# Optimization experiments

Hardware: AMD Instinct MI355X
Metric: run time of the kernel (lower is better)

The kernel has to match this reference:

```python
import jax, jax.numpy as jnp
import numpy as np

B, T, C, H = 4, 2048, 1024, 16
HD = C // H


def setup_inputs() -> dict:
    key = jax.random.key(0)
    ks = jax.random.split(key, 9)
    s = 1.0 / np.sqrt(C)
    return {
        "x": jax.random.normal(ks[0], (B, T, C), dtype=jnp.float32),
        "Wk": jax.random.uniform(ks[1], (C, C), jnp.float32, -s, s),
        "bk": jax.random.uniform(ks[2], (C,), jnp.float32, -s, s),
        "Wq": jax.random.uniform(ks[3], (C, C), jnp.float32, -s, s),
        "bq": jax.random.uniform(ks[4], (C,), jnp.float32, -s, s),
        "Wv": jax.random.uniform(ks[5], (C, C), jnp.float32, -s, s),
        "bv": jax.random.uniform(ks[6], (C,), jnp.float32, -s, s),
        "Wp": jax.random.uniform(ks[7], (C, C), jnp.float32, -s, s),
        "bp": jax.random.uniform(ks[8], (C,), jnp.float32, -s, s),
        "padding_mask": jnp.ones((B, T), dtype=jnp.int32),
    }


def reference(x, Wk, bk, Wq, bq, Wv, bv, Wp, bp, padding_mask):
    # torch nn.Linear: y = x @ W.T + b  (W is [out, in])
    def split_heads(t):  # [B,T,C] -> [B,H,T,HD]
        return t.reshape(B, T, H, HD).transpose(0, 2, 1, 3)

    k = split_heads(x @ Wk.T + bk)
    q = split_heads(x @ Wq.T + bq)
    v = split_heads(x @ Wv.T + bv)

    scale = 1.0 / jnp.sqrt(jnp.float32(HD))
    att = jnp.einsum("bhqd,bhkd->bhqk", q, k) * scale  # [B,H,T,T]

    causal = jnp.tril(jnp.ones((T, T), dtype=bool))  # [T,T]
    pad = (padding_mask != 0)[:, None, None, :]       # [B,1,1,T]
    mask = causal[None, None, :, :] & pad
    att = jnp.where(mask, att, -jnp.inf)
    att = jax.nn.softmax(att, axis=-1)

    y = jnp.einsum("bhqk,bhkd->bhqd", att, v)  # [B,H,T,HD]
    y = y.transpose(0, 2, 1, 3).reshape(B, T, C)
    return y @ Wp.T + bp
```

## Files before the change

kernel.cpp:

```cpp
#include <hip/hip_runtime.h>
#include <hip/hip_bf16.h>
#include <math.h>
#include <stdint.h>

#define BB 4
#define TT 2048
#define CC 1024
#define HH 16
#define HD 64
#define MM (BB*TT)
#define NQT 16
#define SCQ 0.180336878f

using f32x4  = __attribute__((ext_vector_type(4))) float;
using bf16x4 = __attribute__((ext_vector_type(4))) __bf16;
using bf16x8 = __attribute__((ext_vector_type(8))) __bf16;

__device__ __forceinline__ float fast_exp2(float x) {
  return __builtin_amdgcn_exp2f(x);
}

__device__ __forceinline__ void gload_lds16(const void* g, void* l) {
  __builtin_amdgcn_global_load_lds(
      (__attribute__((address_space(1))) void*)(void*)(g),
      (__attribute__((address_space(3))) void*)(l), 16, 0, 0);
}

__global__ __launch_bounds__(256)
void cvt_f32_bf16(const float* __restrict__ s, __bf16* __restrict__ d, int n4) {
  int i = blockIdx.x * 256 + threadIdx.x;
  if (i >= n4) return;
  float4 v = ((const float4*)s)[i];
  bf16x4 o;
  o[0] = (__bf16)v.x; o[1] = (__bf16)v.y; o[2] = (__bf16)v.z; o[3] = (__bf16)v.w;
  *(bf16x4*)(d + (size_t)i * 4) = o;
}

__global__ __launch_bounds__(256)
void cvt_w4(const float* __restrict__ Wq, const float* __restrict__ Wk,
            const float* __restrict__ Wv, const float* __restrict__ Wp,
            __bf16* __restrict__ wqkv, __bf16* __restrict__ wpb) {
  int which = blockIdx.y;
  const float* s = which == 0 ? Wq : which == 1 ? Wk : which == 2 ? Wv : Wp;
  __bf16* d = which == 3 ? wpb : wqkv + (size_t)which * CC * CC;
  float sc = which == 0 ? SCQ : 1.f;
  int i = blockIdx.x * 256 + threadIdx.x;
  float4 v = ((const float4*)s)[i];
  bf16x4 o;
  o[0] = (__bf16)(v.x * sc); o[1] = (__bf16)(v.y * sc);
  o[2] = (__bf16)(v.z * sc); o[3] = (__bf16)(v.w * sc);
  *(bf16x4*)(d + (size_t)i * 4) = o;
}

#define WAITV6 asm volatile("s_waitcnt vmcnt(6)" ::: "memory")
#define WAITV0 asm volatile("s_waitcnt vmcnt(0)" ::: "memory")
#define WAITL0 asm volatile("s_waitcnt lgkmcnt(0)" ::: "memory")
#define BARR   __builtin_amdgcn_s_barrier()
#define SB0    __builtin_amdgcn_sched_barrier(0)
#define PRIO1  __builtin_amdgcn_s_setprio(1)
#define PRIO0  __builtin_amdgcn_s_setprio(0)

#define LDA_SET(buf, mq)                                                      \
  {                                                                           \
    const char* base_ = (const char*)&LA[buf][mq][0] + (wm * 64 + lq) * 128;  \
    _Pragma("unroll")                                                         \
    for (int m4 = 0; m4 < 4; ++m4)                                            \
      _Pragma("unroll")                                                       \
      for (int kk = 0; kk < 2; ++kk)                                          \
        a[m4 * 2 + kk] =                                                      \
            *(const bf16x8*)(base_ + m4 * 2048 + ((kk * 64 + g * 16) ^ swz)); \
  }

#define LDB_SET(buf, nq)                                                      \
  {                                                                           \
    const char* base_ = (const char*)&LB[buf][nq][0] + (wn * 32 + lq) * 128;  \
    _Pragma("unroll")                                                         \
    for (int n2 = 0; n2 < 2; ++n2)                                            \
      _Pragma("unroll")                                                       \
      for (int kk = 0; kk < 2; ++kk)                                          \
        b[nq][n2 * 2 + kk] =                                                  \
            *(const bf16x8*)(base_ + n2 * 2048 + ((kk * 64 + g * 16) ^ swz)); \
  }

#define STAGE_A(nbuf, h, tt)                                                  \
  {                                                                           \
    const char* s_ = Ag + ((size_t)((h)*128 + srow)) * 2048 + (tt)*128 + scol1; \
    gload_lds16(s_, (char*)&LA[nbuf][h][0] + so16);                           \
    gload_lds16(s_ + (size_t)64 * 2048, (char*)&LA[nbuf][h][0] + so16 + 8192);\
  }

#define STAGE_B(nbuf, h, tt)                                                  \
  {                                                                           \
    const char* s_ = Bg + ((size_t)((h)*128 + srow)) * 2048 + (tt)*128 + scol1; \
    gload_lds16(s_, (char*)&LB[nbuf][h][0] + so16);                           \
    gload_lds16(s_ + (size_t)64 * 2048, (char*)&LB[nbuf][h][0] + so16 + 8192);\
  }

#define MFMA_PH(mq, nq)                                                       \
  _Pragma("unroll")                                                           \
  for (int m4 = 0; m4 < 4; ++m4)                                              \
    _Pragma("unroll")                                                         \
    for (int n2 = 0; n2 < 2; ++n2)                                            \
      _Pragma("unroll")                                                       \
      for (int kk = 0; kk < 2; ++kk)                                          \
        acc[mq][m4][nq][n2] = __builtin_amdgcn_mfma_f32_16x16x32_bf16(        \
            a[m4 * 2 + kk], b[nq][n2 * 2 + kk], acc[mq][m4][nq][n2], 0, 0, 0);

__global__ __launch_bounds__(512, 2)
void gemm_qkv(const __bf16* __restrict__ A, const __bf16* __restrict__ Bm,
              const float* __restrict__ b0, const float* __restrict__ b1,
              const float* __restrict__ b2, __bf16* __restrict__ out,
              __bf16* __restrict__ vt) {
  __shared__ __bf16 LA[2][2][128 * 64];
  __shared__ __bf16 LB[2][2][128 * 64];
  const int tid = threadIdx.x, wid = tid >> 6, lane = tid & 63;
  const int g = lane >> 4, lq = lane & 15;
  const int wm = wid >> 2, wn = wid & 3;
  const int bm = blockIdx.x / 12, bn = blockIdx.x % 12;
  const int brow = bm << 8, bcol = bn << 8;
  const int swz = (lq & 7) << 4;

  const int srow = tid >> 3, so16 = tid * 16;
  const int scol1 = ((tid & 7) << 4) ^ ((srow & 7) << 4);
  const char* Ag = (const char*)A + (size_t)brow * 2048;
  const char* Bg = (const char*)Bm + (size_t)bcol * 2048;

  f32x4 acc[2][4][2][2] = {};
  bf16x8 a[8], b[2][4];

  STAGE_A(0, 0, 0); STAGE_B(0, 0, 0); STAGE_B(0, 1, 0); STAGE_A(0, 1, 0);
  STAGE_A(1, 0, 1); STAGE_B(1, 0, 1); STAGE_B(1, 1, 1);
  WAITV6; BARR;

#pragma unroll 1
  for (int t = 0; t < 8; ++t) {
    const bool s2 = (t < 7);
    const int k1 = 2 * t + 1, k2 = 2 * t + 2, k3 = 2 * t + 3;
    LDA_SET(0, 0); LDB_SET(0, 0);
    STAGE_A(1, 1, k1);
    BARR; WAITL0; SB0;
    PRIO1; MFMA_PH(0, 0); PRIO0; BARR;
    LDB_SET(0, 1);
    if (s2) STAGE_A(0, 0, k2);
    BARR; WAITL0; SB0;
    PRIO1; MFMA_PH(0, 1); PRIO0; BARR;
    LDA_SET(0, 1);
    if (s2) STAGE_B(0, 0, k2);
    BARR; WAITL0; SB0;
    PRIO1; MFMA_PH(1, 1); PRIO0; BARR;
    if (s2) { STAGE_B(0, 1, k2); WAITV6; } else { WAITV0; }
    BARR; SB0;
    PRIO1; MFMA_PH(1, 0); PRIO0; BARR;
    LDA_SET(1, 0); LDB_SET(1, 0);
    if (s2) STAGE_A(0, 1, k2);
    BARR; WAITL0; SB0;
    PRIO1; MFMA_PH(0, 0); PRIO0; BARR;
    LDB_SET(1, 1);
    if (s2) STAGE_A(1, 0, k3);
    BARR; WAITL0; SB0;
    PRIO1; MFMA_PH(0, 1); PRIO0; BARR;
    LDA_SET(1, 1);
    if (s2) STAGE_B(1, 0, k3);
    BARR; WAITL0; SB0;
    PRIO1; MFMA_PH(1, 1); PRIO0; BARR;
    if (s2) { STAGE_B(1, 1, k3); WAITV6; }
    BARR; SB0;
    PRIO1; MFMA_PH(1, 0); PRIO0; BARR;
  }

  const int proj = bn >> 2;
  if (proj < 2) {
    const float* bias = proj == 0 ? b0 : b1;
    const float bsc = proj == 0 ? SCQ : 1.f;
#pragma unroll
    for (int mq = 0; mq < 2; ++mq)
#pragma unroll
      for (int nq = 0; nq < 2; ++nq)
#pragma unroll
        for (int n2 = 0; n2 < 2; ++n2) {
          int col = bcol + nq * 128 + wn * 32 + n2 * 16 + lq;
          int cw = col & (CC - 1);
          float bb = bias[cw] * bsc;
          int h_ = cw >> 6, d_ = cw & (HD - 1);
#pragma unroll
          for (int m4 = 0; m4 < 4; ++m4) {
            int row0 = brow + mq * 128 + wm * 64 + m4 * 16 + g * 4;
#pragma unroll
            for (int i = 0; i < 4; ++i) {
              int row = row0 + i;
              int b_ = row >> 11, t_ = row & (TT - 1);
              out[((size_t)proj << 23) +
                  ((((size_t)b_ * HH + h_) * TT + t_) << 6) + d_] =
                  (__bf16)(acc[mq][m4][nq][n2][i] + bb);
            }
          }
        }
  } else {
    __bf16* lt = (__bf16*)&LA[0][0][0];
    const int cv0 = (bn & 3) << 8;
    const int b_ = brow >> 11, t0 = brow & (TT - 1);
    const int hbase = (bn & 3) << 2;
    const int rd_d = tid >> 3, rd_tb = (tid & 7) << 5;
#pragma unroll
    for (int cc = 0; cc < 4; ++cc) {
      if ((wn >> 1) == (cc & 1)) {
#pragma unroll
        for (int n2 = 0; n2 < 2; ++n2) {
          int c = ((wn & 1) << 5) + (n2 << 4) + lq;
          float bb = b2[cv0 + (cc << 6) + c];
#pragma unroll
          for (int mq = 0; mq < 2; ++mq)
#pragma unroll
            for (int m4 = 0; m4 < 4; ++m4) {
              int r = (mq << 7) + (wm << 6) + (m4 << 4) + (g << 2);
              bf16x4 pk;
#pragma unroll
              for (int i = 0; i < 4; ++i)
                pk[i] = (__bf16)(acc[mq][m4][cc >> 1][n2][i] + bb);
              *(bf16x4*)(lt + c * 264 + r) = pk;
            }
        }
      }
      __syncthreads();
      __bf16* dst = vt + (((size_t)((b_ * HH + hbase + cc) * HD + rd_d)) << 11)
                       + t0 + rd_tb;
      const __bf16* srcl = lt + rd_d * 264 + rd_tb;
#pragma unroll
      for (int j = 0; j < 4; ++j)
        *(bf16x8*)(dst + j * 8) = *(const bf16x8*)(srcl + j * 8);
      __syncthreads();
    }
  }
}

__global__ __launch_bounds__(256, 2)
void gemm_proj(const __bf16* __restrict__ A, const __bf16* __restrict__ Bm,
               const float* __restrict__ bias, float* __restrict__ out,
               int M, int N, int K) {
  __shared__ __bf16 As[128 * 32];
  __shared__ __bf16 Bs[128 * 32];
  const int tid = threadIdx.x;
  const int wid = tid >> 6, lane = tid & 63;
  const int g = lane >> 4, lq = lane & 15;
  const int nbn = N >> 7;
  const int brow = (blockIdx.x / nbn) << 7;
  const int bcol = (blockIdx.x % nbn) << 7;
  const int wr = (wid >> 1) << 6, wc = (wid & 1) << 6;

  f32x4 acc[4][4] = {};

  const int o0 = wid * 2048 + lane * 16;
  for (int kt = 0; kt < K; kt += 32) {
    __syncthreads();
#pragma unroll
    for (int j = 0; j < 2; ++j) {
      int o = o0 + j * 1024;
      int row = o >> 6, colb = o & 63;
      gload_lds16((const char*)A + ((size_t)(brow + row) * K + kt) * 2 + colb,
                  (char*)As + o);
      gload_lds16((const char*)Bm + ((size_t)(bcol + row) * K + kt) * 2 + colb,
                  (char*)Bs + o);
    }
    __syncthreads();
    bf16x8 av[4], bv[4];
#pragma unroll
    for (int m = 0; m < 4; ++m)
      av[m] = *(const bf16x8*)(As + (wr + m * 16 + lq) * 32 + g * 8);
#pragma unroll
    for (int n = 0; n < 4; ++n)
      bv[n] = *(const bf16x8*)(Bs + (wc + n * 16 + lq) * 32 + g * 8);
#pragma unroll
    for (int m = 0; m < 4; ++m)
#pragma unroll
      for (int n = 0; n < 4; ++n)
        acc[m][n] = __builtin_amdgcn_mfma_f32_16x16x32_bf16(av[m], bv[n], acc[m][n], 0, 0, 0);
  }

#pragma unroll
  for (int m = 0; m < 4; ++m) {
#pragma unroll
    for (int n = 0; n < 4; ++n) {
      int col = bcol + wc + n * 16 + lq;
      float bb = bias[col];
      int row0 = brow + wr + m * 16 + g * 4;
#pragma unroll
      for (int i = 0; i < 4; ++i)
        out[(size_t)(row0 + i) * N + col] = acc[m][n][i] + bb;
    }
  }
}

__global__ __launch_bounds__(512, 6)
void attn_fwd(const __bf16* __restrict__ Q, const __bf16* __restrict__ K,
              const __bf16* __restrict__ Vt, const int* __restrict__ pm,
              __bf16* __restrict__ Y) {
  __shared__ __bf16 Ks[2][64 * 64];
  __shared__ __bf16 Vs[2][64 * 64];
  __shared__ __bf16 Ps[8][16 * 72];
  const int tid = threadIdx.x, wid = tid >> 6, lane = tid & 63;
  const int g = lane >> 4, lq = lane & 15;
  const int bx = blockIdx.x;
  const int bh = bx & 63, jj = bx >> 6;
  const int qi = (jj & 1) ? ((jj - 1) >> 1) : (NQT - 1 - (jj >> 1));
  const int b_ = bh >> 4, h_ = bh & 15;
  const __bf16* Qb = Q + (size_t)bh * TT * HD;
  const __bf16* Kb = K + (size_t)bh * TT * HD;
  const __bf16* Vb = Vt + (size_t)bh * HD * TT;
  const int* pmb = pm + b_ * TT;

  const int so = tid * 16;
  const int srow = so >> 7, scol = (so & 127) ^ ((srow & 7) << 4);

  const int q0 = qi << 7;
  const int qw = q0 + wid * 16;
  const int ntiles = 2 * qi + 2;

  bf16x8 qf[2];
#pragma unroll
  for (int s = 0; s < 2; ++s)
    qf[s] = *(const bf16x8*)(Qb + (size_t)(qw + lq) * HD + s * 32 + g * 8);

  bf16x8 ones;
#pragma unroll
  for (int e = 0; e < 8; ++e) ones[e] = (__bf16)1.0f;

  f32x4 o[4] = {};
  f32x4 lacc = {0.f, 0.f, 0.f, 0.f};
  float mrow[4] = {-INFINITY, -INFINITY, -INFINITY, -INFINITY};

  gload_lds16((const char*)Kb + (size_t)srow * 128 + scol, (char*)&Ks[0][0] + so);
  gload_lds16((const char*)Vb + (size_t)srow * (TT * 2) + scol, (char*)&Vs[0][0] + so);
  __syncthreads();

  int cur = 0;
#pragma unroll 1
  for (int t = 0; t < ntiles; ++t) {
    const int kv0 = t << 6;
    const int pmv = pmb[kv0 + lane];
    if (t + 1 < ntiles) {
      const size_t nkv0 = (size_t)(kv0 + 64);
      gload_lds16((const char*)Kb + (nkv0 + srow) * 128 + scol,
                  (char*)&Ks[cur ^ 1][0] + so);
      gload_lds16((const char*)Vb + (size_t)srow * (TT * 2) + nkv0 * 2 + scol,
                  (char*)&Vs[cur ^ 1][0] + so);
    }

    if (kv0 <= qw + 15) {
      unsigned long long bits = __ballot(pmv != 0);

      const char* KsC = (const char*)&Ks[cur][0];
      f32x4 sa[4] = {};
      __builtin_amdgcn_s_setprio(1);
#pragma unroll
      for (int f = 0; f < 4; ++f) {
        int row = 16 * f + lq, sw = (row & 7) << 4;
#pragma unroll
        for (int s = 0; s < 2; ++s) {
          bf16x8 kf = *(const bf16x8*)(KsC + row * 128 + ((s * 64 + g * 16) ^ sw));
          sa[f] = __builtin_amdgcn_mfma_f32_16x16x32_bf16(qf[s], kf, sa[f], 0, 0, 0);
        }
      }
      __builtin_amdgcn_s_setprio(0);

      const bool diag = (kv0 + 63 > qw);
      const bool nopad = (bits == ~0ull);
      float pv_[4][4];
      if (nopad && !diag) {
#pragma unroll
        for (int f = 0; f < 4; ++f)
#pragma unroll
          for (int i = 0; i < 4; ++i) pv_[f][i] = sa[f][i];
      } else {
#pragma unroll
        for (int f = 0; f < 4; ++f) {
          int kvf = 16 * f + lq;
          float cm = ((bits >> kvf) & 1ull) ? 0.f : -INFINITY;
          int kv = kv0 + kvf;
#pragma unroll
          for (int i = 0; i < 4; ++i) {
            float s = sa[f][i] + cm;
            if (diag) s = (kv <= qw + 4 * g + i) ? s : -INFINITY;
            pv_[f][i] = s;
          }
        }
      }

      float pmax[4];
#pragma unroll
      for (int i = 0; i < 4; ++i)
        pmax[i] = fmaxf(fmaxf(pv_[0][i], pv_[1][i]), fmaxf(pv_[2][i], pv_[3][i]));
      bool ok = (pmax[0] <= mrow[0] + 8.f) && (pmax[1] <= mrow[1] + 8.f) &&
                (pmax[2] <= mrow[2] + 8.f) && (pmax[3] <= mrow[3] + 8.f);
      if (!__all(ok)) {
        float nmax[4] = {pmax[0], pmax[1], pmax[2], pmax[3]};
#pragma unroll
        for (int d = 1; d < 16; d <<= 1)
#pragma unroll
          for (int i = 0; i < 4; ++i)
            nmax[i] = fmaxf(nmax[i], __shfl_xor(nmax[i], d));
#pragma unroll
        for (int i = 0; i < 4; ++i) {
          float mn = fmaxf(mrow[i], nmax[i]);
          float c = fast_exp2(mrow[i] - mn);
          mrow[i] = mn;
          lacc[i] *= c;
#pragma unroll
          for (int fd = 0; fd < 4; ++fd) o[fd][i] *= c;
        }
      }

#pragma unroll
      for (int f = 0; f < 4; ++f)
#pragma unroll
        for (int i = 0; i < 4; ++i)
          Ps[wid][(4 * g + i) * 72 + 16 * f + lq] =
              (__bf16)fast_exp2(pv_[f][i] - mrow[i]);

      const char* VsC = (const char*)&Vs[cur][0];
      __builtin_amdgcn_s_setprio(1);
#pragma unroll
      for (int s = 0; s < 2; ++s) {
        bf16x8 pa = *(const bf16x8*)(&Ps[wid][0] + lq * 72 + s * 32 + g * 8);
        lacc = __builtin_amdgcn_mfma_f32_16x16x32_bf16(pa, ones, lacc, 0, 0, 0);
#pragma unroll
        for (int fd = 0; fd < 4; ++fd) {
          int row = 16 * fd + lq;
          bf16x8 vf = *(const bf16x8*)(VsC + row * 128 +
                                       ((s * 64 + g * 16) ^ ((row & 7) << 4)));
          o[fd] = __builtin_amdgcn_mfma_f32_16x16x32_bf16(pa, vf, o[fd], 0, 0, 0);
        }
      }
      __builtin_amdgcn_s_setprio(0);
    }

    __syncthreads();
    cur ^= 1;
  }

  float inv[4];
#pragma unroll
  for (int i = 0; i < 4; ++i) inv[i] = 1.f / lacc[i];
#pragma unroll
  for (int fd = 0; fd < 4; ++fd)
#pragma unroll
    for (int i = 0; i < 4; ++i) {
      int qrow = qw + 4 * g + i;
      Y[((size_t)(b_ * TT + qrow)) * CC + h_ * HD + 16 * fd + lq] =
          (__bf16)(o[fd][i] * inv[i]);
    }
}

extern "C" void kernel_launch(void* const* d_in, const int* in_sizes, int n_in,
                              void* d_out, int out_size, void* d_ws, size_t ws_size,
                              hipStream_t stream) {
  (void)in_sizes; (void)n_in; (void)out_size; (void)ws_size;
  const float* x  = (const float*)d_in[0];
  const float* Wk = (const float*)d_in[1];
  const float* bk = (const float*)d_in[2];
  const float* Wq = (const float*)d_in[3];
  const float* bq = (const float*)d_in[4];
  const float* Wv = (const float*)d_in[5];
  const float* bv = (const float*)d_in[6];
  const float* Wp = (const float*)d_in[7];
  const float* bp = (const float*)d_in[8];
  const int* pmask = (const int*)d_in[9];

  char* ws = (char*)d_ws;
  const size_t MB = 1024 * 1024;
  __bf16* xb   = (__bf16*)(ws);
  __bf16* wqkv = (__bf16*)(ws + 16 * MB);
  __bf16* wpb  = (__bf16*)(ws + 22 * MB);
  __bf16* qb   = (__bf16*)(ws + 24 * MB);
  __bf16* kb   = qb + ((size_t)1 << 23);
  __bf16* vtb  = (__bf16*)(ws + 56 * MB);
  __bf16* yb   = xb;

  int n4 = (MM * CC) / 4;
  cvt_f32_bf16<<<(n4 + 255) / 256, 256, 0, stream>>>(x, xb, n4);
  cvt_w4<<<dim3((CC * CC / 4) / 256, 4), 256, 0, stream>>>(
      Wq, Wk, Wv, Wp, wqkv, wpb);

  gemm_qkv<<<(MM / 256) * (3 * CC / 256), 512, 0, stream>>>(
      xb, wqkv, bq, bk, bv, qb, vtb);

  attn_fwd<<<NQT * BB * HH, 512, 0, stream>>>(qb, kb, vtb, pmask, yb);

  gemm_proj<<<(MM / 128) * (CC / 128), 256, 0, stream>>>(
      yb, wpb, bp, (float*)d_out, MM, CC, CC);
}
```

Baseline: 184.9 us.

## Rewrite attention inner loop with 32x32 MFMA and register-resident P

Switches the attention kernel from 16x16x32 MFMA tiles to 32x32x16 MFMA tiles, computing S transposed (K×Q) so each lane owns one query row. The softmax probabilities stay in registers, packed to bf16 and exchanged across lane halves with shuffles, instead of going through an LDS staging buffer. The row sum is accumulated with VALU adds instead of an extra MFMA against ones. Each wave now handles 32 query rows (256 per block, 8 query tiles), and occupancy hints drop from 6 to 4 to allow the higher register use.

```diff
diff --git a/kernel.cpp b/kernel.cpp
--- a/kernel.cpp
+++ b/kernel.cpp
@@ -9,15 +9,23 @@
 #define HH 16
 #define HD 64
 #define MM (BB*TT)
-#define NQT 16
+#define NQT 8
 #define SCQ 0.180336878f
 
 using f32x4  = __attribute__((ext_vector_type(4))) float;
+using f32x16 = __attribute__((ext_vector_type(16))) float;
+using i32x4  = __attribute__((ext_vector_type(4))) int;
 using bf16x4 = __attribute__((ext_vector_type(4))) __bf16;
 using bf16x8 = __attribute__((ext_vector_type(8))) __bf16;
 
 __device__ __forceinline__ float fast_exp2(float x) {
   return __builtin_amdgcn_exp2f(x);
+}
+
+__device__ __forceinline__ int cvt_pk_bf16(float lo, float hi_) {
+  int r;
+  asm("v_cvt_pk_bf16_f32 %0, %1, %2" : "=v"(r) : "v"(lo), "v"(hi_));
+  return r;
 }
 
 __device__ __forceinline__ void gload_lds16(const void* g, void* l) {
@@ -290,18 +298,18 @@
   }
 }
 
-__global__ __launch_bounds__(512, 6)
+__global__ __launch_bounds__(512, 4)
 void attn_fwd(const __bf16* __restrict__ Q, const __bf16* __restrict__ K,
               const __bf16* __restrict__ Vt, const int* __restrict__ pm,
               __bf16* __restrict__ Y) {
   __shared__ __bf16 Ks[2][64 * 64];
   __shared__ __bf16 Vs[2][64 * 64];
-  __shared__ __bf16 Ps[8][16 * 72];
   const int tid = threadIdx.x, wid = tid >> 6, lane = tid & 63;
-  const int g = lane >> 4, lq = lane & 15;
+  const int l31 = lane & 31, hi = lane >> 5;
   const int bx = blockIdx.x;
   const int bh = bx & 63, jj = bx >> 6;
-  const int qi = (jj & 1) ? ((jj - 1) >> 1) : (NQT - 1 - (jj >> 1));
+  const int r2 = ((jj & 1) << 1) | ((jj >> 1) & 1);
+  const int qi = (jj & 4) ? r2 : 7 - r2;
   const int b_ = bh >> 4, h_ = bh & 15;
   const __bf16* Qb = Q + (size_t)bh * TT * HD;
   const __bf16* Kb = K + (size_t)bh * TT * HD;
@@ -311,22 +319,19 @@
   const int so = tid * 16;
   const int srow = so >> 7, scol = (so & 127) ^ ((srow & 7) << 4);
 
-  const int q0 = qi << 7;
-  const int qw = q0 + wid * 16;
-  const int ntiles = 2 * qi + 2;
-
-  bf16x8 qf[2];
-#pragma unroll
-  for (int s = 0; s < 2; ++s)
-    qf[s] = *(const bf16x8*)(Qb + (size_t)(qw + lq) * HD + s * 32 + g * 8);
-
-  bf16x8 ones;
-#pragma unroll
-  for (int e = 0; e < 8; ++e) ones[e] = (__bf16)1.0f;
-
-  f32x4 o[4] = {};
-  f32x4 lacc = {0.f, 0.f, 0.f, 0.f};
-  float mrow[4] = {-INFINITY, -INFINITY, -INFINITY, -INFINITY};
+  const int q0 = qi << 8;
+  const int qw = q0 + wid * 32;
+  const int ntiles = 4 * qi + 4;
+  const int sw0 = (l31 & 7) << 4;
+
+  bf16x8 qf[4];
+#pragma unroll
+  for (int s = 0; s < 4; ++s)
+    qf[s] = *(const bf16x8*)(Qb + (size_t)(qw + l31) * HD + s * 16 + hi * 8);
+
+  f32x16 o0 = {}, o1 = {};
+  float lsum = 0.f;
+  float m = -INFINITY;
 
   gload_lds16((const char*)Kb + (size_t)srow * 128 + scol, (char*)&Ks[0][0] + so);
   gload_lds16((const char*)Vb + (size_t)srow * (TT * 2) + scol, (char*)&Vs[0][0] + so);
@@ -345,90 +350,102 @@
                   (char*)&Vs[cur ^ 1][0] + so);
     }
 
-    if (kv0 <= qw + 15) {
+    if (kv0 <= qw + 31) {
       unsigned long long bits = __ballot(pmv != 0);
 
       const char* KsC = (const char*)&Ks[cur][0];
-      f32x4 sa[4] = {};
+      f32x16 sA = {}, sB = {};
       __builtin_amdgcn_s_setprio(1);
 #pragma unroll
-      for (int f = 0; f < 4; ++f) {
-        int row = 16 * f + lq, sw = (row & 7) << 4;
-#pragma unroll
-        for (int s = 0; s < 2; ++s) {
-          bf16x8 kf = *(const bf16x8*)(KsC + row * 128 + ((s * 64 + g * 16) ^ sw));
-          sa[f] = __builtin_amdgcn_mfma_f32_16x16x32_bf16(qf[s], kf, sa[f], 0, 0, 0);
-        }
+      for (int s = 0; s < 4; ++s) {
+        const int co = 32 * s + 16 * hi;
+        bf16x8 k0 = *(const bf16x8*)(KsC + l31 * 128 + (co ^ sw0));
+        bf16x8 k1 = *(const bf16x8*)(KsC + (32 + l31) * 128 + (co ^ sw0));
+        sA = __builtin_amdgcn_mfma_f32_32x32x16_bf16(k0, qf[s], sA, 0, 0, 0);
+        sB = __builtin_amdgcn_mfma_f32_32x32x16_bf16(k1, qf[s], sB, 0, 0, 0);
       }
       __builtin_amdgcn_s_setprio(0);
 
       const bool diag = (kv0 + 63 > qw);
       const bool nopad = (bits == ~0ull);
-      float pv_[4][4];
-      if (nopad && !diag) {
-#pragma unroll
-        for (int f = 0; f < 4; ++f)
-#pragma unroll
-          for (int i = 0; i < 4; ++i) pv_[f][i] = sa[f][i];
-      } else {
-#pragma unroll
-        for (int f = 0; f < 4; ++f) {
-          int kvf = 16 * f + lq;
-          float cm = ((bits >> kvf) & 1ull) ? 0.f : -INFINITY;
-          int kv = kv0 + kvf;
-#pragma unroll
-          for (int i = 0; i < 4; ++i) {
-            float s = sa[f][i] + cm;
-            if (diag) s = (kv <= qw + 4 * g + i) ? s : -INFINITY;
-            pv_[f][i] = s;
-          }
+      if (__builtin_expect(!nopad, 0)) {
+#pragma unroll
+        for (int r = 0; r < 16; ++r) {
+          const int c = (r & 3) + 8 * (r >> 2);
+          if (!((bits >> (c + 4 * hi)) & 1ull)) sA[r] = -INFINITY;
+          if (!((bits >> (32 + c + 4 * hi)) & 1ull)) sB[r] = -INFINITY;
         }
       }
-
-      float pmax[4];
-#pragma unroll
-      for (int i = 0; i < 4; ++i)
-        pmax[i] = fmaxf(fmaxf(pv_[0][i], pv_[1][i]), fmaxf(pv_[2][i], pv_[3][i]));
-      bool ok = (pmax[0] <= mrow[0] + 8.f) && (pmax[1] <= mrow[1] + 8.f) &&
-                (pmax[2] <= mrow[2] + 8.f) && (pmax[3] <= mrow[3] + 8.f);
+      if (diag) {
+        const int thr = qw + l31 - kv0 - 4 * hi;
+#pragma unroll
+        for (int r = 0; r < 16; ++r) {
+          const int c = (r & 3) + 8 * (r >> 2);
+          sA[r] = (c <= thr) ? sA[r] : -INFINITY;
+          sB[r] = (32 + c <= thr) ? sB[r] : -INFINITY;
+        }
+      }
+
+      float mx[8];
+#pragma unroll
+      for (int r = 0; r < 8; ++r)
+        mx[r] = fmaxf(fmaxf(sA[r], sA[r + 8]), fmaxf(sB[r], sB[r + 8]));
+#pragma unroll
+      for (int r = 0; r < 4; ++r) mx[r] = fmaxf(mx[r], mx[r + 4]);
+      float pmax = fmaxf(fmaxf(mx[0], mx[1]), fmaxf(mx[2], mx[3]));
+
+      const bool ok = (pmax <= m + 8.f);
       if (!__all(ok)) {
-        float nmax[4] = {pmax[0], pmax[1], pmax[2], pmax[3]};
-#pragma unroll
-        for (int d = 1; d < 16; d <<= 1)
-#pragma unroll
-          for (int i = 0; i < 4; ++i)
-            nmax[i] = fmaxf(nmax[i], __shfl_xor(nmax[i], d));
-#pragma unroll
-        for (int i = 0; i < 4; ++i) {
-          float mn = fmaxf(mrow[i], nmax[i]);
-          float c = fast_exp2(mrow[i] - mn);
-          mrow[i] = mn;
-          lacc[i] *= c;
-#pragma unroll
-          for (int fd = 0; fd < 4; ++fd) o[fd][i] *= c;
+        float nm = fmaxf(pmax, __shfl_xor(pmax, 32));
+        float mn = fmaxf(m, nm);
+        float c = fast_exp2(m - mn);
+        m = mn;
+        lsum *= c;
+#pragma unroll
+        for (int r = 0; r < 16; ++r) {
+          float cr = __shfl(c, (r & 3) + 8 * (r >> 2) + 4 * hi);
+          o0[r] *= cr;
+          o1[r] *= cr;
         }
       }
 
 #pragma unroll
-      for (int f = 0; f < 4; ++f)
-#pragma unroll
-        for (int i = 0; i < 4; ++i)
-          Ps[wid][(4 * g + i) * 72 + 16 * f + lq] =
-              (__bf16)fast_exp2(pv_[f][i] - mrow[i]);
+      for (int r = 0; r < 16; ++r) sA[r] = fast_exp2(sA[r] - m);
+#pragma unroll
+      for (int r = 0; r < 16; ++r) sB[r] = fast_exp2(sB[r] - m);
+      {
+        float sm[8];
+#pragma unroll
+        for (int r = 0; r < 8; ++r)
+          sm[r] = (sA[r] + sA[r + 8]) + (sB[r] + sB[r + 8]);
+#pragma unroll
+        for (int r = 0; r < 4; ++r) sm[r] += sm[r + 4];
+        lsum += (sm[0] + sm[1]) + (sm[2] + sm[3]);
+      }
 
       const char* VsC = (const char*)&Vs[cur][0];
       __builtin_amdgcn_s_setprio(1);
 #pragma unroll
-      for (int s = 0; s < 2; ++s) {
-        bf16x8 pa = *(const bf16x8*)(&Ps[wid][0] + lq * 72 + s * 32 + g * 8);
-        lacc = __builtin_amdgcn_mfma_f32_16x16x32_bf16(pa, ones, lacc, 0, 0, 0);
-#pragma unroll
-        for (int fd = 0; fd < 4; ++fd) {
-          int row = 16 * fd + lq;
-          bf16x8 vf = *(const bf16x8*)(VsC + row * 128 +
-                                       ((s * 64 + g * 16) ^ ((row & 7) << 4)));
-          o[fd] = __builtin_amdgcn_mfma_f32_16x16x32_bf16(pa, vf, o[fd], 0, 0, 0);
-        }
+      for (int s = 0; s < 4; ++s) {
+        const f32x16& P = (s < 2) ? sA : sB;
+        const int ub = 2 * (s & 1);
+        int A0 = cvt_pk_bf16(P[4 * ub + 0], P[4 * ub + 1]);
+        int A1 = cvt_pk_bf16(P[4 * ub + 2], P[4 * ub + 3]);
+        int B0 = cvt_pk_bf16(P[4 * ub + 4], P[4 * ub + 5]);
+        int B1 = cvt_pk_bf16(P[4 * ub + 6], P[4 * ub + 7]);
+        int s0 = hi ? A0 : B0, s1 = hi ? A1 : B1;
+        int e0 = __shfl_xor(s0, 32), e1 = __shfl_xor(s1, 32);
+        i32x4 wv;
+        wv[0] = hi ? e0 : A0;
+        wv[1] = hi ? e1 : A1;
+        wv[2] = hi ? B0 : e0;
+        wv[3] = hi ? B1 : e1;
+        bf16x8 pa = __builtin_bit_cast(bf16x8, wv);
+        const int co = 32 * s + 16 * hi;
+        bf16x8 v0 = *(const bf16x8*)(VsC + l31 * 128 + (co ^ sw0));
+        bf16x8 v1 = *(const bf16x8*)(VsC + (32 + l31) * 128 + (co ^ sw0));
+        o0 = __builtin_amdgcn_mfma_f32_32x32x16_bf16(pa, v0, o0, 0, 0, 0);
+        o1 = __builtin_amdgcn_mfma_f32_32x32x16_bf16(pa, v1, o1, 0, 0, 0);
       }
       __builtin_amdgcn_s_setprio(0);
     }
@@ -437,17 +454,16 @@
     cur ^= 1;
   }
 
-  float inv[4];
-#pragma unroll
-  for (int i = 0; i < 4; ++i) inv[i] = 1.f / lacc[i];
-#pragma unroll
-  for (int fd = 0; fd < 4; ++fd)
-#pragma unroll
-    for (int i = 0; i < 4; ++i) {
-      int qrow = qw + 4 * g + i;
-      Y[((size_t)(b_ * TT + qrow)) * CC + h_ * HD + 16 * fd + lq] =
-          (__bf16)(o[fd][i] * inv[i]);
-    }
+  float linv = 1.f / (lsum + __shfl_xor(lsum, 32));
+#pragma unroll
+  for (int r = 0; r < 16; ++r) {
+    const int crow = (r & 3) + 8 * (r >> 2) + 4 * hi;
+    float ir = __shfl(linv, crow);
+    const int qrow = qw + crow;
+    __bf16* yp = Y + ((size_t)(b_ * TT + qrow)) * CC + h_ * HD + l31;
+    yp[0]  = (__bf16)(o0[r] * ir);
+    yp[32] = (__bf16)(o1[r] * ir);
+  }
 }
 
 extern "C" void kernel_launch(void* const* d_in, const int* in_sizes, int n_in,
```

Result: no change. 182.5 us (-1.3%).
